# Kernel tuning notes

Measured on AMD Instinct MI355X. Metric: run time of the kernel, lower is better.

The kernel has to match this reference:

```python
import jax, jax.numpy as jnp
import numpy as np

N = 50000       # nodes
E = 800000      # edges (before self-loops)
G = 64          # graphs in batch
F_IN = 128      # node_features
HID = 64        # hidden_channels
H1 = 8          # conv1 heads
NEG_SLOPE = 0.2
EPS = 1e-16


def _gat_layer(x, src, dst, W, att_src, att_dst, bias, heads, out_ch, concat):
    """PyG GATConv (eval mode: dropout inactive). src/dst include self-loops.
    x: [N, F_in]; W: [F_in, heads*out_ch]; att_*: [heads, out_ch]; bias: [heads*out_ch] or [out_ch]."""
    n = x.shape[0]
    h = (x @ W).reshape(n, heads, out_ch)                 # [N,H,C]
    a_s = jnp.sum(h * att_src, axis=-1)                   # [N,H]
    a_d = jnp.sum(h * att_dst, axis=-1)                   # [N,H]
    e = jax.nn.leaky_relu(a_s[src] + a_d[dst], NEG_SLOPE)  # [Etot,H]
    # segment softmax over incoming edges of each destination node
    m = jax.ops.segment_max(e, dst, num_segments=n)       # [N,H]
    e = jnp.exp(e - m[dst])
    denom = jax.ops.segment_sum(e, dst, num_segments=n)   # [N,H]
    alpha = e / (denom[dst] + EPS)                        # [Etot,H]
    msg = h[src] * alpha[:, :, None]                      # [Etot,H,C]
    out = jax.ops.segment_sum(msg, dst, num_segments=n)   # [N,H,C]
    if concat:
        out = out.reshape(n, heads * out_ch)
    else:
        out = out.mean(axis=1)
    return out + bias


def setup_inputs() -> dict:
    key = jax.random.key(0)
    ks = jax.random.split(key, 14)
    x = jax.random.normal(ks[0], (N, F_IN), dtype=jnp.float32)
    edge_index = jax.random.randint(ks[1], (2, E), 0, N, dtype=jnp.int64)
    batch_index = jnp.sort(jax.random.randint(ks[2], (N,), 0, G, dtype=jnp.int64))
    s = 0.05
    return {
        "x": x,
        "edge_index": edge_index,
        "batch_index": batch_index,
        "W1": jax.random.normal(ks[3], (F_IN, H1 * HID), dtype=jnp.float32) * s,
        "att_src1": jax.random.normal(ks[4], (H1, HID), dtype=jnp.float32) * s,
        "att_dst1": jax.random.normal(ks[5], (H1, HID), dtype=jnp.float32) * s,
        "b1": jnp.zeros((H1 * HID,), dtype=jnp.float32),
        "W2": jax.random.normal(ks[6], (H1 * HID, HID), dtype=jnp.float32) * s,
        "att_src2": jax.random.normal(ks[7], (1, HID), dtype=jnp.float32) * s,
        "att_dst2": jax.random.normal(ks[8], (1, HID), dtype=jnp.float32) * s,
        "b2": jnp.zeros((HID,), dtype=jnp.float32),
        "lin_W": jax.random.normal(ks[9], (HID, 1), dtype=jnp.float32) * s,
        "lin_b": jnp.zeros((1,), dtype=jnp.float32),
    }


def reference(x, edge_index, batch_index, W1, att_src1, att_dst1, b1,
              W2, att_src2, att_dst2, b2, lin_W, lin_b):
    n = x.shape[0]
    loops = jnp.arange(n, dtype=edge_index.dtype)
    src = jnp.concatenate([edge_index[0], loops])
    dst = jnp.concatenate([edge_index[1], loops])
    # eval mode: F.dropout is identity
    h = jax.nn.elu(_gat_layer(x, src, dst, W1, att_src1, att_dst1, b1, H1, HID, True))
    h = _gat_layer(h, src, dst, W2, att_src2, att_dst2, b2, 1, HID, False)
    # global mean pool over graphs
    sums = jax.ops.segment_sum(h, batch_index, num_segments=G)          # [G,HID]
    cnt = jax.ops.segment_sum(jnp.ones((n,), h.dtype), batch_index, num_segments=G)
    pooled = sums / jnp.maximum(cnt, 1.0)[:, None]
    return pooled @ lin_W + lin_b                                       # [G,1]
```

## Files before the change

### kernel.cpp

```cpp
#include <hip/hip_runtime.h>
#include <math.h>

#define NN 50000
#define EE 800000
#define ET 850000
#define GG 64
#define MPAD 50048
#define NCAP 64
#define NROW 50016
#define CSRI (NROW * NCAP)
#define CSTRIDE 32

typedef __attribute__((ext_vector_type(8))) short bf16x8;
typedef __attribute__((ext_vector_type(4))) float f32x4;

__device__ __forceinline__ float lrelu(float v) { return v > 0.f ? v : 0.2f * v; }

__device__ __forceinline__ unsigned short f2bf(float f) {
  unsigned u = __float_as_uint(f);
  u += 0x7FFFu + ((u >> 16) & 1u);
  return (unsigned short)(u >> 16);
}
__device__ __forceinline__ unsigned pack2(float a, float b) {
  return (unsigned)f2bf(a) | ((unsigned)f2bf(b) << 16);
}
__device__ __forceinline__ void bfacc4(uint4 u, float a, float* o) {
  o[0] += a * __uint_as_float(u.x << 16);
  o[1] += a * __uint_as_float(u.x & 0xFFFF0000u);
  o[2] += a * __uint_as_float(u.y << 16);
  o[3] += a * __uint_as_float(u.y & 0xFFFF0000u);
  o[4] += a * __uint_as_float(u.z << 16);
  o[5] += a * __uint_as_float(u.z & 0xFFFF0000u);
  o[6] += a * __uint_as_float(u.w << 16);
  o[7] += a * __uint_as_float(u.w & 0xFFFF0000u);
}

#define INIT_BLOCKS 1563
#define CVT_X_BLOCKS 3128
#define CVT_W_BLOCKS 256
#define V_BLOCKS 2
#define GSEG_BLOCKS 196
__global__ __launch_bounds__(256) void prep_kernel(const float* __restrict__ x,
                                                   const float* __restrict__ W1,
                                                   const float* __restrict__ W2,
                                                   const float* __restrict__ att_s2,
                                                   const float* __restrict__ att_d2,
                                                   const float* __restrict__ linW,
                                                   const int* __restrict__ batch,
                                                   unsigned short* __restrict__ xb,
                                                   unsigned short* __restrict__ W1T,
                                                   float* __restrict__ Vs,
                                                   float* __restrict__ Vd,
                                                   float* __restrict__ Vz,
                                                   int* __restrict__ gstart,
                                                   int* __restrict__ cursor,
                                                   unsigned short* __restrict__ csr) {
  int b = blockIdx.x;
  if (b < INIT_BLOCKS) {
    int i = b * 256 + threadIdx.x;
    if (i < CSRI / 8) {
      uint4 sf = {0xC350C350u, 0xC350C350u, 0xC350C350u, 0xC350C350u};
      ((uint4*)csr)[i] = sf;
    }
    if (i < NROW) cursor[i * CSTRIDE] = 0;
  } else if (b < INIT_BLOCKS + CVT_X_BLOCKS) {
    int i8 = (b - INIT_BLOCKS) * 256 + threadIdx.x;
    if (i8 >= MPAD * 128 / 8) return;
    size_t e0 = (size_t)i8 * 8;
    int row = (int)(e0 >> 7);
    uint4 o;
    if (row < NN) {
      float4 f0 = *(const float4*)(x + e0);
      float4 f1 = *(const float4*)(x + e0 + 4);
      o.x = pack2(f0.x, f0.y); o.y = pack2(f0.z, f0.w);
      o.z = pack2(f1.x, f1.y); o.w = pack2(f1.z, f1.w);
    } else {
      o.x = o.y = o.z = o.w = 0u;
    }
    *(uint4*)(xb + e0) = o;
  } else if (b < INIT_BLOCKS + CVT_X_BLOCKS + CVT_W_BLOCKS) {
    int i = (b - INIT_BLOCKS - CVT_X_BLOCKS) * 256 + threadIdx.x;
    int k = i >> 9, n = i & 511;
    W1T[n * 128 + k] = f2bf(W1[i]);
  } else if (b < INIT_BLOCKS + CVT_X_BLOCKS + CVT_W_BLOCKS + V_BLOCKS) {
    int k = (b - INIT_BLOCKS - CVT_X_BLOCKS - CVT_W_BLOCKS) * 256 + threadIdx.x;
    float vs = 0.f, vd = 0.f, vz = 0.f;
#pragma unroll 8
    for (int c = 0; c < 64; ++c) {
      float w = W2[k * 64 + c];
      vs += w * att_s2[c];
      vd += w * att_d2[c];
      vz += w * linW[c];
    }
    Vs[k] = vs; Vd[k] = vd; Vz[k] = vz;
  } else {
    int e = (b - INIT_BLOCKS - CVT_X_BLOCKS - CVT_W_BLOCKS - V_BLOCKS) * 256 + threadIdx.x;
    if (e < NN) {
      int bb = batch[e];
      if (e == 0) {
        for (int g = 0; g <= bb; ++g) gstart[g] = 0;
      } else {
        int pb = batch[e - 1];
        for (int g = pb + 1; g <= bb; ++g) gstart[g] = e;
      }
      if (e == NN - 1) {
        for (int g = bb + 1; g <= GG; ++g) gstart[g] = NN;
      }
    }
  }
}

#define GEMM_BLOCKS 3128
#define SCAT_BLOCKS 831
#define SCAT_STRIDE (SCAT_BLOCKS * 256)
__global__ __launch_bounds__(256) void gemm1_scatter(const unsigned short* __restrict__ xb,
                                                     const unsigned short* __restrict__ W1T,
                                                     const float* __restrict__ att_s,
                                                     const float* __restrict__ att_d,
                                                     unsigned short* __restrict__ h1b,
                                                     float* __restrict__ as1,
                                                     float* __restrict__ ad1,
                                                     const int* __restrict__ ei,
                                                     int* __restrict__ cursor,
                                                     unsigned short* __restrict__ csr) {
  __shared__ unsigned short st[2][64 * 72];
  const int idx = blockIdx.x;
  const bool is_scat = ((idx & 3) == 3) && ((idx >> 2) < SCAT_BLOCKS);
  if (is_scat) {
    int base = (idx >> 2) * 256 + threadIdx.x;
#pragma unroll
    for (int k = 0; k < 4; ++k) {
      int e = base + k * SCAT_STRIDE;
      if (e < ET) {
        int src = (e < EE) ? ei[e] : (e - EE);
        int dst = (e < EE) ? ei[EE + e] : (e - EE);
        int pos = atomicAdd(&cursor[dst * CSTRIDE], 1);
        if (pos < NCAP) csr[dst * NCAP + pos] = (unsigned short)src;
      }
    }
    return;
  }
  const int gi = idx - min((idx + 1) >> 2, SCAT_BLOCKS);

  const int t = threadIdx.x, w = t >> 6, l = t & 63;
  const int bm = (gi >> 2) * 64;
  const int ypair = gi & 3;
  const int m16 = l & 15, q = l >> 4;
  const int row = bm + w * 16 + m16;

  const bf16x8* Ap = (const bf16x8*)(xb + (size_t)row * 128 + q * 8);
  bf16x8 a0 = Ap[0], a1 = Ap[4], a2 = Ap[8], a3 = Ap[12];

  const int r2 = t >> 2, c16 = (t & 3) * 16;

#pragma unroll
  for (int hh = 0; hh < 2; ++hh) {
    const int h = ypair * 2 + hh;
    const bf16x8* Bp = (const bf16x8*)(W1T + (size_t)(h * 64 + m16) * 128 + q * 8);
    f32x4 acc[4] = {};
#pragma unroll
    for (int c = 0; c < 4; ++c) {
      acc[c] = __builtin_amdgcn_mfma_f32_16x16x32_bf16(a0, Bp[(size_t)c * 256 + 0],  acc[c], 0, 0, 0);
      acc[c] = __builtin_amdgcn_mfma_f32_16x16x32_bf16(a1, Bp[(size_t)c * 256 + 4],  acc[c], 0, 0, 0);
      acc[c] = __builtin_amdgcn_mfma_f32_16x16x32_bf16(a2, Bp[(size_t)c * 256 + 8],  acc[c], 0, 0, 0);
      acc[c] = __builtin_amdgcn_mfma_f32_16x16x32_bf16(a3, Bp[(size_t)c * 256 + 12], acc[c], 0, 0, 0);
    }

    float ps[4] = {0.f, 0.f, 0.f, 0.f}, pd[4] = {0.f, 0.f, 0.f, 0.f};
#pragma unroll
    for (int c = 0; c < 4; ++c) {
      float ws = att_s[h * 64 + m16 + 16 * c];
      float wd = att_d[h * 64 + m16 + 16 * c];
#pragma unroll
      for (int r = 0; r < 4; ++r) {
        ps[r] += acc[c][r] * ws;
        pd[r] += acc[c][r] * wd;
      }
    }
#pragma unroll
    for (int off = 1; off < 16; off <<= 1) {
#pragma unroll
      for (int r = 0; r < 4; ++r) {
        ps[r] += __shfl_xor(ps[r], off);
        pd[r] += __shfl_xor(pd[r], off);
      }
    }
    if (m16 == 0) {
#pragma unroll
      for (int r = 0; r < 4; ++r) {
        int rr = bm + w * 16 + q * 4 + r;
        as1[rr * 8 + h] = (rr < NN) ? ps[r] : -1e30f;
        ad1[rr * 8 + h] = (rr < NN) ? pd[r] : 0.f;
      }
    }

#pragma unroll
    for (int c = 0; c < 4; ++c)
#pragma unroll
      for (int r = 0; r < 4; ++r)
        st[hh][(w * 16 + q * 4 + r) * 72 + m16 + 16 * c] = f2bf(acc[c][r]);
    __syncthreads();
    uint4* dst = (uint4*)(h1b + (size_t)(bm + r2) * 512 + h * 64 + c16);
    const uint4* srcp = (const uint4*)(st[hh] + r2 * 72 + c16);
    dst[0] = srcp[0];
    dst[1] = srcp[1];
  }
}

#define ISSUE8(K, U0, U1, U2, U3, U4, U5, U6, U7, ASV) do {                  \
    uint4 cc;                                                                \
    cc.x = __shfl(cb.x, (K)); cc.y = __shfl(cb.y, (K));                      \
    cc.z = __shfl(cb.z, (K)); cc.w = __shfl(cb.w, (K));                      \
    unsigned pr = (slot_a & 4) ? ((slot_a & 2) ? cc.w : cc.z)                \
                               : ((slot_a & 2) ? cc.y : cc.x);               \
    int my_src = (slot_a & 1) ? (int)(pr >> 16) : (int)(pr & 0xFFFFu);       \
    ASV = as1[my_src * 8 + ha];                                              \
    int s0 = (int)(cc.x & 0xFFFFu), s1 = (int)(cc.x >> 16);                  \
    int s2 = (int)(cc.y & 0xFFFFu), s3 = (int)(cc.y >> 16);                  \
    int s4 = (int)(cc.z & 0xFFFFu), s5 = (int)(cc.z >> 16);                  \
    int s6 = (int)(cc.w & 0xFFFFu), s7 = (int)(cc.w >> 16);                  \
    U0 = *(const uint4*)(h1b + (size_t)s0 * 512 + lane * 8);                 \
    U1 = *(const uint4*)(h1b + (size_t)s1 * 512 + lane * 8);                 \
    U2 = *(const uint4*)(h1b + (size_t)s2 * 512 + lane * 8);                 \
    U3 = *(const uint4*)(h1b + (size_t)s3 * 512 + lane * 8);                 \
    U4 = *(const uint4*)(h1b + (size_t)s4 * 512 + lane * 8);                 \
    U5 = *(const uint4*)(h1b + (size_t)s5 * 512 + lane * 8);                 \
    U6 = *(const uint4*)(h1b + (size_t)s6 * 512 + lane * 8);                 \
    U7 = *(const uint4*)(h1b + (size_t)s7 * 512 + lane * 8);                 \
  } while (0)

#define PROC8(U0, U1, U2, U3, U4, U5, U6, U7, ASV) do {                      \
    float myal = __expf(lrelu((ASV) + adv_a));                               \
    float a0 = __shfl(myal, hb + 0), a1 = __shfl(myal, hb + 1);              \
    float a2 = __shfl(myal, hb + 2), a3 = __shfl(myal, hb + 3);              \
    float a4 = __shfl(myal, hb + 4), a5 = __shfl(myal, hb + 5);              \
    float a6 = __shfl(myal, hb + 6), a7 = __shfl(myal, hb + 7);              \
    den += ((a0 + a1) + (a2 + a3)) + ((a4 + a5) + (a6 + a7));                \
    bfacc4(U0, a0, o); bfacc4(U1, a1, o);                                    \
    bfacc4(U2, a2, o); bfacc4(U3, a3, o);                                    \
    bfacc4(U4, a4, o); bfacc4(U5, a5, o);                                    \
    bfacc4(U6, a6, o); bfacc4(U7, a7, o);                                    \
  } while (0)

__global__ __launch_bounds__(256) void agg1_kernel(const unsigned short* __restrict__ h1b,
                                                   const float* __restrict__ as1,
                                                   const float* __restrict__ ad1,
                                                   const int* __restrict__ cnt,
                                                   const unsigned short* __restrict__ csr,
                                                   const float* __restrict__ b1,
                                                   const float* __restrict__ Vs,
                                                   const float* __restrict__ Vd,
                                                   const float* __restrict__ Vz,
                                                   float* __restrict__ as2,
                                                   float* __restrict__ ad2,
                                                   float* __restrict__ zz) {
  int dst = blockIdx.x * 4 + (threadIdx.x >> 6);
  int lane = threadIdx.x & 63;
  if (dst >= NN) return;
  const int ha = lane >> 3;
  const int hb = ha * 8;
  const int slot_a = lane & 7;

  const int cv = min(cnt[dst * CSTRIDE], NCAP);
  const uint4 cb = *(const uint4*)(csr + dst * NCAP + (lane & 7) * 8);
  const float adv_a = ad1[dst * 8 + ha];
  const int nb = (cv + 7) >> 3;

  float den = 0.f;
  float o[8] = {0.f, 0.f, 0.f, 0.f, 0.f, 0.f, 0.f, 0.f};
  uint4 A0, A1, A2, A3, A4, A5, A6, A7;
  uint4 B0, B1, B2, B3, B4, B5, B6, B7;
  float asA, asB;

  ISSUE8(0, A0, A1, A2, A3, A4, A5, A6, A7, asA);
  int k = 0;
  for (;;) {
    if (k + 1 < nb) ISSUE8(k + 1, B0, B1, B2, B3, B4, B5, B6, B7, asB);
    PROC8(A0, A1, A2, A3, A4, A5, A6, A7, asA);
    if (++k >= nb) break;
    if (k + 1 < nb) ISSUE8(k + 1, A0, A1, A2, A3, A4, A5, A6, A7, asA);
    PROC8(B0, B1, B2, B3, B4, B5, B6, B7, asB);
    if (++k >= nb) break;
  }
  float inv = 1.0f / (den + 1e-16f);

  const float4* bp = (const float4*)(b1 + lane * 8);
  float4 bb0 = bp[0], bb1 = bp[1];
  float bb[8] = {bb0.x, bb0.y, bb0.z, bb0.w, bb1.x, bb1.y, bb1.z, bb1.w};
  float v[8];
#pragma unroll
  for (int j = 0; j < 8; ++j) {
    float t = o[j] * inv + bb[j];
    v[j] = (t > 0.f) ? t : (__expf(t) - 1.0f);
  }

  const float4* vsp = (const float4*)(Vs + lane * 8);
  const float4* vdp = (const float4*)(Vd + lane * 8);
  const float4* vzp = (const float4*)(Vz + lane * 8);
  float4 vs0 = vsp[0], vs1 = vsp[1];
  float4 vd0 = vdp[0], vd1 = vdp[1];
  float4 vz0 = vzp[0], vz1 = vzp[1];
  float ps = v[0]*vs0.x + v[1]*vs0.y + v[2]*vs0.z + v[3]*vs0.w
           + v[4]*vs1.x + v[5]*vs1.y + v[6]*vs1.z + v[7]*vs1.w;
  float pd = v[0]*vd0.x + v[1]*vd0.y + v[2]*vd0.z + v[3]*vd0.w
           + v[4]*vd1.x + v[5]*vd1.y + v[6]*vd1.z + v[7]*vd1.w;
  float pz = v[0]*vz0.x + v[1]*vz0.y + v[2]*vz0.z + v[3]*vz0.w
           + v[4]*vz1.x + v[5]*vz1.y + v[6]*vz1.z + v[7]*vz1.w;
#pragma unroll
  for (int off = 1; off < 64; off <<= 1) {
    ps += __shfl_xor(ps, off);
    pd += __shfl_xor(pd, off);
    pz += __shfl_xor(pz, off);
  }
  if (lane == 0) {
    as2[dst] = ps;
    ad2[dst] = pd;
    zz[dst]  = pz;
  }
}

__global__ __launch_bounds__(256) void agg2z_kernel(const float* __restrict__ as2,
                                                    const float* __restrict__ ad2,
                                                    const float* __restrict__ z,
                                                    const int* __restrict__ cnt,
                                                    const unsigned short* __restrict__ csr,
                                                    float* __restrict__ s) {
  int dst = blockIdx.x * 4 + (threadIdx.x >> 6);
  int lane = threadIdx.x & 63;
  if (dst >= NN) return;
  const int si = dst * NCAP, e = si + cnt[dst * CSTRIDE];
  const float adv = ad2[dst];
  float num = 0.f, den = 0.f;
  for (int i = si + lane; i < e; i += 64) {
    int src = csr[i];
    float a = __expf(lrelu(as2[src] + adv));
    num += a * z[src];
    den += a;
  }
#pragma unroll
  for (int off = 32; off > 0; off >>= 1) {
    num += __shfl_xor(num, off);
    den += __shfl_xor(den, off);
  }
  if (lane == 0) s[dst] = num / (den + 1e-16f);
}

__global__ __launch_bounds__(256) void poolz_kernel(const float* __restrict__ s,
                                                    const int* __restrict__ gstart,
                                                    const float* __restrict__ b2,
                                                    const float* __restrict__ linW,
                                                    const float* __restrict__ linb,
                                                    float* __restrict__ out) {
  __shared__ float red[4];
  int g = blockIdx.x;
  int t = threadIdx.x, lane = t & 63, w = t >> 6;
  int s0 = gstart[g], e0 = gstart[g + 1];
  float acc = 0.f;
  for (int i = s0 + t; i < e0; i += 256) acc += s[i];
#pragma unroll
  for (int off = 32; off > 0; off >>= 1) acc += __shfl_xor(acc, off);
  if (lane == 0) red[w] = acc;
  __syncthreads();
  if (w == 0) {
    float total = red[0] + red[1] + red[2] + red[3];
    float bz = b2[lane] * linW[lane];
#pragma unroll
    for (int off = 32; off > 0; off >>= 1) bz += __shfl_xor(bz, off);
    if (lane == 0) {
      float cnt = fmaxf((float)(e0 - s0), 1.0f);
      out[g] = total / cnt + bz + linb[0];
    }
  }
}

extern "C" void kernel_launch(void* const* d_in, const int* in_sizes, int n_in,
                              void* d_out, int out_size, void* d_ws, size_t ws_size,
                              hipStream_t stream) {
  const float* x      = (const float*)d_in[0];
  const int*   ei     = (const int*)d_in[1];
  const int*   batch  = (const int*)d_in[2];
  const float* W1     = (const float*)d_in[3];
  const float* att_s1 = (const float*)d_in[4];
  const float* att_d1 = (const float*)d_in[5];
  const float* b1     = (const float*)d_in[6];
  const float* W2     = (const float*)d_in[7];
  const float* att_s2 = (const float*)d_in[8];
  const float* att_d2 = (const float*)d_in[9];
  const float* b2     = (const float*)d_in[10];
  const float* linW   = (const float*)d_in[11];
  const float* linb   = (const float*)d_in[12];
  float* out = (float*)d_out;

  char* base = (char*)d_ws;
  unsigned short* xb  = (unsigned short*)base; base += (size_t)MPAD * 128 * 2;
  unsigned short* h1b = (unsigned short*)base; base += (size_t)MPAD * 512 * 2;
  unsigned short* W1T = (unsigned short*)base; base += (size_t)512 * 128 * 2;
  float* Vs   = (float*)base; base += (size_t)512 * 4;
  float* Vd   = (float*)base; base += (size_t)512 * 4;
  float* Vz   = (float*)base; base += (size_t)512 * 4;
  float* as1  = (float*)base; base += (size_t)MPAD * 8 * 4;
  float* ad1  = (float*)base; base += (size_t)MPAD * 8 * 4;
  float* as2  = (float*)base; base += (size_t)NROW * 4;
  float* ad2  = (float*)base; base += (size_t)NROW * 4;
  float* zz   = (float*)base; base += (size_t)NROW * 4;
  float* sv   = (float*)base; base += (size_t)NROW * 4;
  int* cursor = (int*)base;  base += (size_t)NROW * CSTRIDE * 4;
  unsigned short* csr = (unsigned short*)base; base += (size_t)CSRI * 2;
  int* gstart = (int*)base;  base += (size_t)(GG + 16) * 4;

  if (ws_size < (size_t)(base - (char*)d_ws)) return;

  prep_kernel<<<INIT_BLOCKS + CVT_X_BLOCKS + CVT_W_BLOCKS + V_BLOCKS + GSEG_BLOCKS,
                256, 0, stream>>>(x, W1, W2, att_s2, att_d2, linW, batch,
                                  xb, W1T, Vs, Vd, Vz, gstart, cursor, csr);

  gemm1_scatter<<<GEMM_BLOCKS + SCAT_BLOCKS, 256, 0, stream>>>(
      xb, W1T, att_s1, att_d1, h1b, as1, ad1, ei, cursor, csr);

  agg1_kernel<<<12500, 256, 0, stream>>>(h1b, as1, ad1, cursor, csr, b1,
                                         Vs, Vd, Vz, as2, ad2, zz);

  agg2z_kernel<<<12500, 256, 0, stream>>>(as2, ad2, zz, cursor, csr, sv);
  poolz_kernel<<<GG, 256, 0, stream>>>(sv, gstart, b2, linW, linb, out);
}
```

Measured before the change: 314.1 us.

## Quantize layer-1 node features to int8 with per-row-head scales for gather

The first GEMM now stores the projected features as int8, with one absmax scale per node and head, in place of bf16. The scale is packed together with the source attention logit into a float2. The aggregation kernel gathers 8-byte int8 rows instead of 16-byte bf16 rows and folds the scale into the attention weight. The aim is to halve the bytes of the bandwidth-bound random gather in agg1, at the cost of int8 quantization error and a little extra dequantization arithmetic.

```diff
diff --git a/kernel.cpp b/kernel.cpp
--- a/kernel.cpp
+++ b/kernel.cpp
@@ -24,15 +24,15 @@
 __device__ __forceinline__ unsigned pack2(float a, float b) {
   return (unsigned)f2bf(a) | ((unsigned)f2bf(b) << 16);
 }
-__device__ __forceinline__ void bfacc4(uint4 u, float a, float* o) {
-  o[0] += a * __uint_as_float(u.x << 16);
-  o[1] += a * __uint_as_float(u.x & 0xFFFF0000u);
-  o[2] += a * __uint_as_float(u.y << 16);
-  o[3] += a * __uint_as_float(u.y & 0xFFFF0000u);
-  o[4] += a * __uint_as_float(u.z << 16);
-  o[5] += a * __uint_as_float(u.z & 0xFFFF0000u);
-  o[6] += a * __uint_as_float(u.w << 16);
-  o[7] += a * __uint_as_float(u.w & 0xFFFF0000u);
+__device__ __forceinline__ void i8acc(uint2 u, float a, float* o) {
+  o[0] += a * (float)((int)(u.x << 24) >> 24);
+  o[1] += a * (float)((int)(u.x << 16) >> 24);
+  o[2] += a * (float)((int)(u.x <<  8) >> 24);
+  o[3] += a * (float)((int)u.x >> 24);
+  o[4] += a * (float)((int)(u.y << 24) >> 24);
+  o[5] += a * (float)((int)(u.y << 16) >> 24);
+  o[6] += a * (float)((int)(u.y <<  8) >> 24);
+  o[7] += a * (float)((int)u.y >> 24);
 }
 
 #define INIT_BLOCKS 1563
@@ -117,13 +117,13 @@
                                                      const unsigned short* __restrict__ W1T,
                                                      const float* __restrict__ att_s,
                                                      const float* __restrict__ att_d,
-                                                     unsigned short* __restrict__ h1b,
-                                                     float* __restrict__ as1,
+                                                     unsigned char* __restrict__ h1i,
+                                                     float2* __restrict__ asc,
                                                      float* __restrict__ ad1,
                                                      const int* __restrict__ ei,
                                                      int* __restrict__ cursor,
                                                      unsigned short* __restrict__ csr) {
-  __shared__ unsigned short st[2][64 * 72];
+  __shared__ unsigned char st8[2][64 * 72];
   const int idx = blockIdx.x;
   const bool is_scat = ((idx & 3) == 3) && ((idx >> 2) < SCAT_BLOCKS);
   if (is_scat) {
@@ -167,6 +167,11 @@
     }
 
     float ps[4] = {0.f, 0.f, 0.f, 0.f}, pd[4] = {0.f, 0.f, 0.f, 0.f};
+    float pm[4];
+#pragma unroll
+    for (int r = 0; r < 4; ++r)
+      pm[r] = fmaxf(fmaxf(fabsf(acc[0][r]), fabsf(acc[1][r])),
+                    fmaxf(fabsf(acc[2][r]), fabsf(acc[3][r])));
 #pragma unroll
     for (int c = 0; c < 4; ++c) {
       float ws = att_s[h * 64 + m16 + 16 * c];
@@ -183,67 +188,80 @@
       for (int r = 0; r < 4; ++r) {
         ps[r] += __shfl_xor(ps[r], off);
         pd[r] += __shfl_xor(pd[r], off);
+        pm[r] = fmaxf(pm[r], __shfl_xor(pm[r], off));
       }
     }
     if (m16 == 0) {
 #pragma unroll
       for (int r = 0; r < 4; ++r) {
         int rr = bm + w * 16 + q * 4 + r;
-        as1[rr * 8 + h] = (rr < NN) ? ps[r] : -1e30f;
+        float2 av;
+        av.x = (rr < NN) ? ps[r] : -1e30f;
+        av.y = pm[r] * (1.0f / 127.0f);
+        asc[rr * 8 + h] = av;
         ad1[rr * 8 + h] = (rr < NN) ? pd[r] : 0.f;
       }
     }
 
+    float invq[4];
+#pragma unroll
+    for (int r = 0; r < 4; ++r)
+      invq[r] = 127.0f * __builtin_amdgcn_rcpf(fmaxf(pm[r], 1e-30f));
 #pragma unroll
     for (int c = 0; c < 4; ++c)
 #pragma unroll
-      for (int r = 0; r < 4; ++r)
-        st[hh][(w * 16 + q * 4 + r) * 72 + m16 + 16 * c] = f2bf(acc[c][r]);
+      for (int r = 0; r < 4; ++r) {
+        int qv = (int)__builtin_rintf(acc[c][r] * invq[r]);
+        st8[hh][(w * 16 + q * 4 + r) * 72 + m16 + 16 * c] = (unsigned char)(qv & 0xFF);
+      }
     __syncthreads();
-    uint4* dst = (uint4*)(h1b + (size_t)(bm + r2) * 512 + h * 64 + c16);
-    const uint4* srcp = (const uint4*)(st[hh] + r2 * 72 + c16);
-    dst[0] = srcp[0];
-    dst[1] = srcp[1];
-  }
-}
-
-#define ISSUE8(K, U0, U1, U2, U3, U4, U5, U6, U7, ASV) do {                  \
+    const unsigned* sp = (const unsigned*)(st8[hh] + r2 * 72 + c16);
+    uint4 o4; o4.x = sp[0]; o4.y = sp[1]; o4.z = sp[2]; o4.w = sp[3];
+    *(uint4*)(h1i + (size_t)(bm + r2) * 512 + h * 64 + c16) = o4;
+  }
+}
+
+#define ISSUE8(K, U0, U1, U2, U3, U4, U5, U6, U7, ASV, SCV) do {             \
     uint4 cc;                                                                \
     cc.x = __shfl(cb.x, (K)); cc.y = __shfl(cb.y, (K));                      \
     cc.z = __shfl(cb.z, (K)); cc.w = __shfl(cb.w, (K));                      \
     unsigned pr = (slot_a & 4) ? ((slot_a & 2) ? cc.w : cc.z)                \
                                : ((slot_a & 2) ? cc.y : cc.x);               \
     int my_src = (slot_a & 1) ? (int)(pr >> 16) : (int)(pr & 0xFFFFu);       \
-    ASV = as1[my_src * 8 + ha];                                              \
+    float2 av = asc[my_src * 8 + ha];                                        \
+    ASV = av.x; SCV = av.y;                                                  \
     int s0 = (int)(cc.x & 0xFFFFu), s1 = (int)(cc.x >> 16);                  \
     int s2 = (int)(cc.y & 0xFFFFu), s3 = (int)(cc.y >> 16);                  \
     int s4 = (int)(cc.z & 0xFFFFu), s5 = (int)(cc.z >> 16);                  \
     int s6 = (int)(cc.w & 0xFFFFu), s7 = (int)(cc.w >> 16);                  \
-    U0 = *(const uint4*)(h1b + (size_t)s0 * 512 + lane * 8);                 \
-    U1 = *(const uint4*)(h1b + (size_t)s1 * 512 + lane * 8);                 \
-    U2 = *(const uint4*)(h1b + (size_t)s2 * 512 + lane * 8);                 \
-    U3 = *(const uint4*)(h1b + (size_t)s3 * 512 + lane * 8);                 \
-    U4 = *(const uint4*)(h1b + (size_t)s4 * 512 + lane * 8);                 \
-    U5 = *(const uint4*)(h1b + (size_t)s5 * 512 + lane * 8);                 \
-    U6 = *(const uint4*)(h1b + (size_t)s6 * 512 + lane * 8);                 \
-    U7 = *(const uint4*)(h1b + (size_t)s7 * 512 + lane * 8);                 \
+    U0 = *(const uint2*)(h1i + (size_t)s0 * 512 + lane * 8);                 \
+    U1 = *(const uint2*)(h1i + (size_t)s1 * 512 + lane * 8);                 \
+    U2 = *(const uint2*)(h1i + (size_t)s2 * 512 + lane * 8);                 \
+    U3 = *(const uint2*)(h1i + (size_t)s3 * 512 + lane * 8);                 \
+    U4 = *(const uint2*)(h1i + (size_t)s4 * 512 + lane * 8);                 \
+    U5 = *(const uint2*)(h1i + (size_t)s5 * 512 + lane * 8);                 \
+    U6 = *(const uint2*)(h1i + (size_t)s6 * 512 + lane * 8);                 \
+    U7 = *(const uint2*)(h1i + (size_t)s7 * 512 + lane * 8);                 \
   } while (0)
 
-#define PROC8(U0, U1, U2, U3, U4, U5, U6, U7, ASV) do {                      \
+#define PROC8(U0, U1, U2, U3, U4, U5, U6, U7, ASV, SCV) do {                 \
     float myal = __expf(lrelu((ASV) + adv_a));                               \
-    float a0 = __shfl(myal, hb + 0), a1 = __shfl(myal, hb + 1);              \
-    float a2 = __shfl(myal, hb + 2), a3 = __shfl(myal, hb + 3);              \
-    float a4 = __shfl(myal, hb + 4), a5 = __shfl(myal, hb + 5);              \
-    float a6 = __shfl(myal, hb + 6), a7 = __shfl(myal, hb + 7);              \
-    den += ((a0 + a1) + (a2 + a3)) + ((a4 + a5) + (a6 + a7));                \
-    bfacc4(U0, a0, o); bfacc4(U1, a1, o);                                    \
-    bfacc4(U2, a2, o); bfacc4(U3, a3, o);                                    \
-    bfacc4(U4, a4, o); bfacc4(U5, a5, o);                                    \
-    bfacc4(U6, a6, o); bfacc4(U7, a7, o);                                    \
+    float d8 = myal;                                                         \
+    d8 += __shfl_xor(d8, 1); d8 += __shfl_xor(d8, 2); d8 += __shfl_xor(d8, 4);\
+    den += d8;                                                               \
+    float ac = myal * (SCV);                                                 \
+    float a0 = __shfl(ac, hb + 0), a1 = __shfl(ac, hb + 1);                  \
+    float a2 = __shfl(ac, hb + 2), a3 = __shfl(ac, hb + 3);                  \
+    float a4 = __shfl(ac, hb + 4), a5 = __shfl(ac, hb + 5);                  \
+    float a6 = __shfl(ac, hb + 6), a7 = __shfl(ac, hb + 7);                  \
+    i8acc(U0, a0, o); i8acc(U1, a1, o);                                      \
+    i8acc(U2, a2, o); i8acc(U3, a3, o);                                      \
+    i8acc(U4, a4, o); i8acc(U5, a5, o);                                      \
+    i8acc(U6, a6, o); i8acc(U7, a7, o);                                      \
   } while (0)
 
-__global__ __launch_bounds__(256) void agg1_kernel(const unsigned short* __restrict__ h1b,
-                                                   const float* __restrict__ as1,
+__global__ __launch_bounds__(256) void agg1_kernel(const unsigned char* __restrict__ h1i,
+                                                   const float2* __restrict__ asc,
                                                    const float* __restrict__ ad1,
                                                    const int* __restrict__ cnt,
                                                    const unsigned short* __restrict__ csr,
@@ -268,18 +286,18 @@
 
   float den = 0.f;
   float o[8] = {0.f, 0.f, 0.f, 0.f, 0.f, 0.f, 0.f, 0.f};
-  uint4 A0, A1, A2, A3, A4, A5, A6, A7;
-  uint4 B0, B1, B2, B3, B4, B5, B6, B7;
-  float asA, asB;
-
-  ISSUE8(0, A0, A1, A2, A3, A4, A5, A6, A7, asA);
+  uint2 A0, A1, A2, A3, A4, A5, A6, A7;
+  uint2 B0, B1, B2, B3, B4, B5, B6, B7;
+  float asA, asB, scA, scB;
+
+  ISSUE8(0, A0, A1, A2, A3, A4, A5, A6, A7, asA, scA);
   int k = 0;
   for (;;) {
-    if (k + 1 < nb) ISSUE8(k + 1, B0, B1, B2, B3, B4, B5, B6, B7, asB);
-    PROC8(A0, A1, A2, A3, A4, A5, A6, A7, asA);
+    if (k + 1 < nb) ISSUE8(k + 1, B0, B1, B2, B3, B4, B5, B6, B7, asB, scB);
+    PROC8(A0, A1, A2, A3, A4, A5, A6, A7, asA, scA);
     if (++k >= nb) break;
-    if (k + 1 < nb) ISSUE8(k + 1, A0, A1, A2, A3, A4, A5, A6, A7, asA);
-    PROC8(B0, B1, B2, B3, B4, B5, B6, B7, asB);
+    if (k + 1 < nb) ISSUE8(k + 1, A0, A1, A2, A3, A4, A5, A6, A7, asA, scA);
+    PROC8(B0, B1, B2, B3, B4, B5, B6, B7, asB, scB);
     if (++k >= nb) break;
   }
   float inv = 1.0f / (den + 1e-16f);
@@ -393,12 +411,12 @@
 
   char* base = (char*)d_ws;
   unsigned short* xb  = (unsigned short*)base; base += (size_t)MPAD * 128 * 2;
-  unsigned short* h1b = (unsigned short*)base; base += (size_t)MPAD * 512 * 2;
+  unsigned char*  h1i = (unsigned char*)base;  base += (size_t)MPAD * 512;
   unsigned short* W1T = (unsigned short*)base; base += (size_t)512 * 128 * 2;
   float* Vs   = (float*)base; base += (size_t)512 * 4;
   float* Vd   = (float*)base; base += (size_t)512 * 4;
   float* Vz   = (float*)base; base += (size_t)512 * 4;
-  float* as1  = (float*)base; base += (size_t)MPAD * 8 * 4;
+  float2* asc = (float2*)base; base += (size_t)MPAD * 8 * 8;
   float* ad1  = (float*)base; base += (size_t)MPAD * 8 * 4;
   float* as2  = (float*)base; base += (size_t)NROW * 4;
   float* ad2  = (float*)base; base += (size_t)NROW * 4;
@@ -415,9 +433,9 @@
                                   xb, W1T, Vs, Vd, Vz, gstart, cursor, csr);
 
   gemm1_scatter<<<GEMM_BLOCKS + SCAT_BLOCKS, 256, 0, stream>>>(
-      xb, W1T, att_s1, att_d1, h1b, as1, ad1, ei, cursor, csr);
-
-  agg1_kernel<<<12500, 256, 0, stream>>>(h1b, as1, ad1, cursor, csr, b1,
+      xb, W1T, att_s1, att_d1, h1i, asc, ad1, ei, cursor, csr);
+
+  agg1_kernel<<<12500, 256, 0, stream>>>(h1i, asc, ad1, cursor, csr, b1,
                                          Vs, Vd, Vz, as2, ad2, zz);
 
   agg2z_kernel<<<12500, 256, 0, stream>>>(as2, ad2, zz, cursor, csr, sv);
```

After: 264.7 us. 15.7% less time.
